# Kernel tuning notes

Hardware: AMD Instinct MI355X
Metric: run time of the kernel (lower is better)

Reference implementation:

```python
import jax, jax.numpy as jnp
import numpy as np

N = 131072      # number of nodes / samples
IN_DIM = 128    # input_dim
H = 128         # hidden_dim
OUT_DIM = 10    # output_dim


def setup_inputs() -> dict:
    key = jax.random.key(0)
    ks = jax.random.split(key, 20)
    s = 0.05
    def rn(k, shape):
        return jax.random.normal(k, shape, jnp.float32) * s
    return {
        "x": jax.random.normal(ks[0], (N, IN_DIM), jnp.float32),
        # GRU layer 1 (seq_len=1, h0=0 => weight_hh contributes nothing; only b_hh matters)
        "w_ih_f1": rn(ks[1], (3 * H, IN_DIM)), "b_ih_f1": rn(ks[2], (3 * H,)), "b_hh_f1": rn(ks[3], (3 * H,)),
        "w_ih_b1": rn(ks[4], (3 * H, IN_DIM)), "b_ih_b1": rn(ks[5], (3 * H,)), "b_hh_b1": rn(ks[6], (3 * H,)),
        # GRU layer 2 (input 2H)
        "w_ih_f2": rn(ks[7], (3 * H, 2 * H)), "b_ih_f2": rn(ks[8], (3 * H,)), "b_hh_f2": rn(ks[9], (3 * H,)),
        "w_ih_b2": rn(ks[10], (3 * H, 2 * H)), "b_ih_b2": rn(ks[11], (3 * H,)), "b_hh_b2": rn(ks[12], (3 * H,)),
        # GCNConv layers
        "w_g1": rn(ks[13], (2 * H, 128)), "b_g1": rn(ks[14], (128,)),
        "w_g2": rn(ks[15], (128, 64)), "b_g2": rn(ks[16], (64,)),
        # final fc
        "w_fc": rn(ks[17], (64, OUT_DIM)), "b_fc": rn(ks[18], (OUT_DIM,)),
    }


def _gru_cell_zero(x, w_ih, b_ih, b_hh):
    # PyTorch GRU cell with h_prev = 0: h' = (1 - z) * n_gate
    gi = x @ w_ih.T + b_ih                    # [n, 3H]
    ir, iz, inn = jnp.split(gi, 3, axis=-1)
    hr, hz, hn = jnp.split(b_hh, 3)
    r = jax.nn.sigmoid(ir + hr)
    z = jax.nn.sigmoid(iz + hz)
    ng = jnp.tanh(inn + r * hn)
    return (1.0 - z) * ng


def _gcn(x, w, b, sources, targets, n):
    # PyG GCNConv: D^{-1/2}(A+I)D^{-1/2} X W + b, self-loops already in edge lists
    xw = x @ w                                 # [n, out]
    deg = jax.ops.segment_sum(jnp.ones(sources.shape[0], x.dtype), targets, num_segments=n)
    dinv = jax.lax.rsqrt(deg)
    norm = dinv[sources] * dinv[targets]       # [E]
    msg = norm[:, None] * xw[sources]          # gather
    return jax.ops.segment_sum(msg, targets, num_segments=n) + b  # scatter-add


def reference(x, w_ih_f1, b_ih_f1, b_hh_f1, w_ih_b1, b_ih_b1, b_hh_b1,
              w_ih_f2, b_ih_f2, b_hh_f2, w_ih_b2, b_ih_b2, b_hh_b2,
              w_g1, b_g1, w_g2, b_g2, w_fc, b_fc):
    n = x.shape[0]
    # seq_len = 1 => bidirectional GRU output is [fwd_cell(x); bwd_cell(x)]
    h1 = jnp.concatenate([_gru_cell_zero(x, w_ih_f1, b_ih_f1, b_hh_f1),
                          _gru_cell_zero(x, w_ih_b1, b_ih_b1, b_hh_b1)], axis=-1)
    h2 = jnp.concatenate([_gru_cell_zero(h1, w_ih_f2, b_ih_f2, b_hh_f2),
                          _gru_cell_zero(h1, w_ih_b2, b_ih_b2, b_hh_b2)], axis=-1)
    # chain graph, both directions, plus self loops (GCNConv adds them)
    src = jnp.arange(n - 1)
    dst = jnp.arange(1, n)
    ar = jnp.arange(n)
    sources = jnp.concatenate([src, dst, ar])
    targets = jnp.concatenate([dst, src, ar])
    g1 = _gcn(h2, w_g1, b_g1, sources, targets, n)   # dropout is identity in eval
    g2 = _gcn(g1, w_g2, b_g2, sources, targets, n)
    return g2 @ w_fc + b_fc
```

## Files before the change

kernel.cpp:

```cpp
#include <hip/hip_runtime.h>
#include <stdint.h>

#define N_NODES 131072
#define HDIM 128

typedef __bf16 bf16x8 __attribute__((ext_vector_type(8)));
typedef float f32x4 __attribute__((ext_vector_type(4)));
typedef unsigned short us8 __attribute__((ext_vector_type(8)));
typedef unsigned short ushort_t;

__device__ __forceinline__ float bf2f(ushort_t u) {
    union { float f; uint32_t i; } v; v.i = ((uint32_t)u) << 16; return v.f;
}
__device__ __forceinline__ ushort_t f2bf(float f) {
    union { float f; uint32_t i; } v; v.f = f;
    uint32_t i = v.i;
    return (ushort_t)((i + 0x7FFFu + ((i >> 16) & 1u)) >> 16);
}

__device__ __forceinline__ void gll16(const ushort_t* g, ushort_t* l) {
    __builtin_amdgcn_global_load_lds(
        (const __attribute__((address_space(1))) uint32_t*)g,
        (__attribute__((address_space(3))) uint32_t*)l, 16, 0, 0);
}

__device__ __forceinline__ bf16x8 ldsw(const ushort_t* base, int R, int g) {
    return *(const bf16x8*)&base[R * 64 + (((g - R) & 7) << 3)];
}

__device__ __forceinline__ float fsig(float x) {
    return __builtin_amdgcn_rcpf(1.0f + __expf(-x));
}
__device__ __forceinline__ float ftanh(float y) {
    float yc = fminf(fmaxf(y, -15.0f), 15.0f);
    float e = __expf(2.0f * yc);
    return (e - 1.0f) * __builtin_amdgcn_rcpf(e + 1.0f);
}

template<int NC>
__device__ __forceinline__ void swz(int b, int& m, int& c) {
    int mhi = b / (8 * NC);
    int rem = b - mhi * (8 * NC);
    c = rem >> 3;
    m = mhi * 8 + (rem & 7);
}

__global__ __launch_bounds__(256) void prep_weights(
    const float* __restrict__ w_f1, const float* __restrict__ w_b1,
    const float* __restrict__ w_f2, const float* __restrict__ w_b2,
    ushort_t* __restrict__ PWF1, ushort_t* __restrict__ PWB1,
    ushort_t* __restrict__ PWF2, ushort_t* __restrict__ PWB2)
{
    int idx = blockIdx.x * 256 + threadIdx.x;
    if (idx < 49152) {
        PWF1[idx] = f2bf(w_f1[idx]);
    } else if (idx < 98304) {
        int j = idx - 49152;  PWB1[j] = f2bf(w_b1[j]);
    } else if (idx < 196608) {
        int j = idx - 98304;  PWF2[j] = f2bf(w_f2[j]);
    } else if (idx < 294912) {
        int j = idx - 196608; PWB2[j] = f2bf(w_b2[j]);
    }
}

__global__ __launch_bounds__(256) void prep_M(
    const float* __restrict__ w_g1, const float* __restrict__ b_g1,
    const float* __restrict__ w_g2, const float* __restrict__ b_g2,
    const float* __restrict__ w_fc, const float* __restrict__ b_fc,
    ushort_t* __restrict__ M16, float* __restrict__ cc)
{
    __shared__ float T1[128][10];
    const int t = threadIdx.x;
    if (t < 128) {
        #pragma unroll
        for (int j = 0; j < 10; ++j) {
            float s = 0.0f;
            for (int k3 = 0; k3 < 64; ++k3) s += w_g2[t * 64 + k3] * w_fc[k3 * 10 + j];
            T1[t][j] = s;
        }
    }
    __syncthreads();
    float m[10];
    #pragma unroll
    for (int j = 0; j < 10; ++j) {
        float s = 0.0f;
        for (int k2 = 0; k2 < 128; ++k2) s += w_g1[t * 128 + k2] * T1[k2][j];
        m[j] = s;
    }
    #pragma unroll
    for (int j = 0; j < 16; ++j)
        M16[j * 256 + t] = (j < 10) ? f2bf(m[j]) : (ushort_t)0;
    if (t < 10) {
        float s1 = 0.0f;
        for (int k2 = 0; k2 < 128; ++k2) s1 += b_g1[k2] * T1[k2][t];
        cc[t] = s1;
        float s2 = 0.0f;
        for (int k3 = 0; k3 < 64; ++k3) s2 += b_g2[k3] * w_fc[k3 * 10 + t];
        cc[16 + t] = s2 + b_fc[t];
    }
}

__global__ __launch_bounds__(256) void xconv(
    const float* __restrict__ x, ushort_t* __restrict__ xb)
{
    int idx = blockIdx.x * 256 + threadIdx.x;
    const float* s = x + (size_t)idx * 8;
    float4 f0 = ((const float4*)s)[0];
    float4 f1 = ((const float4*)s)[1];
    us8 t;
    t[0] = f2bf(f0.x); t[1] = f2bf(f0.y); t[2] = f2bf(f0.z); t[3] = f2bf(f0.w);
    t[4] = f2bf(f1.x); t[5] = f2bf(f1.y); t[6] = f2bf(f1.z); t[7] = f2bf(f1.w);
    *(us8*)&xb[(size_t)idx * 8] = t;
}

template<int K>
__global__ __launch_bounds__(256, 5) void gru_gemm2(
    const ushort_t* __restrict__ A,
    const ushort_t* __restrict__ Wf,
    const ushort_t* __restrict__ Wb,
    const float* __restrict__ bi_f, const float* __restrict__ bh_f,
    const float* __restrict__ bi_b, const float* __restrict__ bh_b,
    ushort_t* __restrict__ Hout)
{
    __shared__ ushort_t As[128 * 64];
    __shared__ ushort_t Bs[96 * 64];
    const int tid = threadIdx.x;
    int mt, comb;
    swz<8>(blockIdx.x, mt, comb);
    const int m0 = mt * 128;
    const int dir = comb >> 2;
    const int j0 = (comb & 3) * 32;
    const ushort_t* W = dir ? Wb : Wf;
    const float* b_ih = dir ? bi_b : bi_f;
    const float* b_hh = dir ? bh_b : bh_f;
    const int coloff = dir << 7;

    const int wv = tid >> 6, lane = tid & 63;
    const int lr = lane & 15, lq = lane >> 4;
    const int tr = tid >> 3, tc = tid & 7;
    const int sc = ((tr + tc) & 7) << 3;

    f32x4 acc[3][2][2];
    #pragma unroll
    for (int g = 0; g < 3; ++g)
        #pragma unroll
        for (int rt = 0; rt < 2; ++rt)
            #pragma unroll
            for (int ct = 0; ct < 2; ++ct)
                #pragma unroll
                for (int e = 0; e < 4; ++e) acc[g][rt][ct][e] = 0.0f;

    for (int t = 0; t < K / 64; ++t) {
        const int k0 = t * 64;
        const ushort_t* ga = A + (size_t)(m0 + tr) * K + k0 + sc;
        #pragma unroll
        for (int i = 0; i < 4; ++i)
            gll16(ga + (size_t)i * 32 * K, &As[(i * 256 + tid) * 8]);
        #pragma unroll
        for (int i = 0; i < 3; ++i) {
            int wr = (i << 7) + j0 + tr;
            gll16(W + (size_t)wr * K + k0 + sc, &Bs[(i * 256 + tid) * 8]);
        }
        __syncthreads();
        #pragma unroll
        for (int kk = 0; kk < 64; kk += 32) {
            const int g8 = (kk >> 3) + lq;
            bf16x8 a0 = ldsw(As, wv * 32 + lr, g8);
            bf16x8 a1 = ldsw(As, wv * 32 + 16 + lr, g8);
            #pragma unroll
            for (int g = 0; g < 3; ++g) {
                #pragma unroll
                for (int ct = 0; ct < 2; ++ct) {
                    bf16x8 b = ldsw(Bs, g * 32 + ct * 16 + lr, g8);
                    acc[g][0][ct] = __builtin_amdgcn_mfma_f32_16x16x32_bf16(a0, b, acc[g][0][ct], 0, 0, 0);
                    acc[g][1][ct] = __builtin_amdgcn_mfma_f32_16x16x32_bf16(a1, b, acc[g][1][ct], 0, 0, 0);
                }
            }
        }
        __syncthreads();
    }

    #pragma unroll
    for (int ct = 0; ct < 2; ++ct) {
        const int j = j0 + ct * 16 + lr;
        const float br  = b_ih[j] + b_hh[j];
        const float bz  = b_ih[HDIM + j] + b_hh[HDIM + j];
        const float bn  = b_ih[2 * HDIM + j];
        const float bhn = b_hh[2 * HDIM + j];
        #pragma unroll
        for (int rt = 0; rt < 2; ++rt) {
            #pragma unroll
            for (int r = 0; r < 4; ++r) {
                const int row = m0 + wv * 32 + rt * 16 + lq * 4 + r;
                float rg = fsig(acc[0][rt][ct][r] + br);
                float zg = fsig(acc[1][rt][ct][r] + bz);
                float ng = ftanh(acc[2][rt][ct][r] + bn + rg * bhn);
                Hout[(size_t)row * 256 + coloff + j] = f2bf((1.0f - zg) * ng);
            }
        }
    }
}

__global__ __launch_bounds__(256, 5) void zgemm(
    const ushort_t* __restrict__ A,
    const ushort_t* __restrict__ M16,
    float* __restrict__ Zc)
{
    __shared__ ushort_t As[128 * 64];
    const int tid = threadIdx.x;
    const int m0 = blockIdx.x * 128;
    const int wv = tid >> 6, lane = tid & 63;
    const int lr = lane & 15, lq = lane >> 4;
    const int tr = tid >> 3, tc = tid & 7;
    const int sc = ((tr + tc) & 7) << 3;

    bf16x8 bfrag[8];
    #pragma unroll
    for (int s = 0; s < 8; ++s)
        bfrag[s] = *(const bf16x8*)&M16[lr * 256 + s * 32 + lq * 8];

    f32x4 acc[2];
    #pragma unroll
    for (int e = 0; e < 4; ++e) { acc[0][e] = 0.0f; acc[1][e] = 0.0f; }

    for (int t = 0; t < 4; ++t) {
        const int k0 = t * 64;
        const ushort_t* ga = A + (size_t)(m0 + tr) * 256 + k0 + sc;
        #pragma unroll
        for (int i = 0; i < 4; ++i)
            gll16(ga + (size_t)i * 32 * 256, &As[(i * 256 + tid) * 8]);
        __syncthreads();
        #pragma unroll
        for (int kk = 0; kk < 64; kk += 32) {
            const int g8 = (kk >> 3) + lq;
            bf16x8 a0 = ldsw(As, wv * 32 + lr, g8);
            bf16x8 a1 = ldsw(As, wv * 32 + 16 + lr, g8);
            bf16x8 b = bfrag[t * 2 + (kk >> 5)];
            acc[0] = __builtin_amdgcn_mfma_f32_16x16x32_bf16(a0, b, acc[0], 0, 0, 0);
            acc[1] = __builtin_amdgcn_mfma_f32_16x16x32_bf16(a1, b, acc[1], 0, 0, 0);
        }
        __syncthreads();
    }

    if (lr < 10) {
        #pragma unroll
        for (int rt = 0; rt < 2; ++rt)
            #pragma unroll
            for (int r = 0; r < 4; ++r) {
                int row = m0 + wv * 32 + rt * 16 + lq * 4 + r;
                Zc[(size_t)row * 10 + lr] = acc[rt][r];
            }
    }
}

__device__ __forceinline__ float dcoef(int i) {
    return (i == 0 || i == N_NODES - 1) ? 0.70710678118654752f : 0.57735026918962576f;
}
template<int FIN>
__global__ __launch_bounds__(256) void stencil10(
    const float* __restrict__ in, float* __restrict__ out,
    const float* __restrict__ cc)
{
    int idx = blockIdx.x * 256 + threadIdx.x;
    int i = idx >> 4, c = idx & 15;
    if (c >= 10) return;
    float di = dcoef(i);
    float s = di * in[(size_t)i * 10 + c];
    float dsum = di;
    if (i > 0)           { float dm = dcoef(i - 1); s += dm * in[(size_t)(i - 1) * 10 + c]; dsum += dm; }
    if (i < N_NODES - 1) { float dp = dcoef(i + 1); s += dp * in[(size_t)(i + 1) * 10 + c]; dsum += dp; }
    float r = di * s;
    if (FIN) r += di * dsum * cc[c] + cc[16 + c];
    out[(size_t)i * 10 + c] = r;
}

extern "C" void kernel_launch(void* const* d_in, const int* in_sizes, int n_in,
                              void* d_out, int out_size, void* d_ws, size_t ws_size,
                              hipStream_t stream) {
    const float* x     = (const float*)d_in[0];
    const float* w_f1  = (const float*)d_in[1];
    const float* bi_f1 = (const float*)d_in[2];
    const float* bh_f1 = (const float*)d_in[3];
    const float* w_b1  = (const float*)d_in[4];
    const float* bi_b1 = (const float*)d_in[5];
    const float* bh_b1 = (const float*)d_in[6];
    const float* w_f2  = (const float*)d_in[7];
    const float* bi_f2 = (const float*)d_in[8];
    const float* bh_f2 = (const float*)d_in[9];
    const float* w_b2  = (const float*)d_in[10];
    const float* bi_b2 = (const float*)d_in[11];
    const float* bh_b2 = (const float*)d_in[12];
    const float* w_g1  = (const float*)d_in[13];
    const float* b_g1  = (const float*)d_in[14];
    const float* w_g2  = (const float*)d_in[15];
    const float* b_g2  = (const float*)d_in[16];
    const float* w_fc  = (const float*)d_in[17];
    const float* b_fc  = (const float*)d_in[18];

    char* ws = (char*)d_ws;
    ushort_t* h1   = (ushort_t*)(ws);
    ushort_t* xb   = (ushort_t*)(ws + 67108864);
    ushort_t* h2   = (ushort_t*)(ws + 67108864);
    float*    Zc   = (float*)(ws);
    float*    u    = (float*)(ws + 8388608);
    ushort_t* PWF1 = (ushort_t*)(ws + 134217728);
    ushort_t* PWB1 = PWF1 + 49152;
    ushort_t* PWF2 = PWB1 + 49152;
    ushort_t* PWB2 = PWF2 + 98304;
    ushort_t* M16  = PWB2 + 98304;
    float*    cc   = (float*)(M16 + 4096);

    prep_weights<<<1152, 256, 0, stream>>>(w_f1, w_b1, w_f2, w_b2,
                                           PWF1, PWB1, PWF2, PWB2);
    prep_M<<<1, 256, 0, stream>>>(w_g1, b_g1, w_g2, b_g2, w_fc, b_fc, M16, cc);
    xconv<<<N_NODES * 16 / 256, 256, 0, stream>>>(x, xb);

    gru_gemm2<128><<<N_NODES / 128 * 8, 256, 0, stream>>>(
        xb, PWF1, PWB1, bi_f1, bh_f1, bi_b1, bh_b1, h1);
    gru_gemm2<256><<<N_NODES / 128 * 8, 256, 0, stream>>>(
        h1, PWF2, PWB2, bi_f2, bh_f2, bi_b2, bh_b2, h2);

    zgemm<<<N_NODES / 128, 256, 0, stream>>>(h2, M16, Zc);
    stencil10<0><<<N_NODES * 16 / 256, 256, 0, stream>>>(Zc, u, cc);
    stencil10<1><<<N_NODES * 16 / 256, 256, 0, stream>>>(u, (float*)d_out, cc);
}
```

Measured before the change: 336.1 us.

## Drop LDS staging in GEMMs, fuse two stencils, vectorize prep_M

The GRU and z GEMMs stop staging tiles in shared memory through global_load_lds plus barriers. Each lane now loads its MFMA fragments straight from global memory and relies on L1/L2 for reuse. The two stencil passes are merged into one 5-point kernel, which removes the intermediate buffer and a launch. prep_M caches w_fc in LDS and uses float4 row loads. Direct global fragment loads can cost more memory traffic and latency because tiles are no longer shared across waves.

```diff
diff --git a/kernel.cpp b/kernel.cpp
--- a/kernel.cpp
+++ b/kernel.cpp
@@ -16,16 +16,6 @@
     union { float f; uint32_t i; } v; v.f = f;
     uint32_t i = v.i;
     return (ushort_t)((i + 0x7FFFu + ((i >> 16) & 1u)) >> 16);
-}
-
-__device__ __forceinline__ void gll16(const ushort_t* g, ushort_t* l) {
-    __builtin_amdgcn_global_load_lds(
-        (const __attribute__((address_space(1))) uint32_t*)g,
-        (__attribute__((address_space(3))) uint32_t*)l, 16, 0, 0);
-}
-
-__device__ __forceinline__ bf16x8 ldsw(const ushort_t* base, int R, int g) {
-    return *(const bf16x8*)&base[R * 64 + (((g - R) & 7) << 3)];
 }
 
 __device__ __forceinline__ float fsig(float x) {
@@ -69,23 +59,39 @@
     const float* __restrict__ w_fc, const float* __restrict__ b_fc,
     ushort_t* __restrict__ M16, float* __restrict__ cc)
 {
+    __shared__ float wfc_s[640];
     __shared__ float T1[128][10];
     const int t = threadIdx.x;
+    for (int i = t; i < 640; i += 256) wfc_s[i] = w_fc[i];
+    __syncthreads();
     if (t < 128) {
-        #pragma unroll
-        for (int j = 0; j < 10; ++j) {
-            float s = 0.0f;
-            for (int k3 = 0; k3 < 64; ++k3) s += w_g2[t * 64 + k3] * w_fc[k3 * 10 + j];
-            T1[t][j] = s;
+        float s[10];
+        #pragma unroll
+        for (int j = 0; j < 10; ++j) s[j] = 0.0f;
+        const float4* row = (const float4*)(w_g2 + t * 64);
+        #pragma unroll
+        for (int k4 = 0; k4 < 16; ++k4) {
+            float4 v = row[k4];
+            #pragma unroll
+            for (int j = 0; j < 10; ++j)
+                s[j] += v.x * wfc_s[(k4 * 4 + 0) * 10 + j] + v.y * wfc_s[(k4 * 4 + 1) * 10 + j]
+                      + v.z * wfc_s[(k4 * 4 + 2) * 10 + j] + v.w * wfc_s[(k4 * 4 + 3) * 10 + j];
         }
+        #pragma unroll
+        for (int j = 0; j < 10; ++j) T1[t][j] = s[j];
     }
     __syncthreads();
     float m[10];
     #pragma unroll
-    for (int j = 0; j < 10; ++j) {
-        float s = 0.0f;
-        for (int k2 = 0; k2 < 128; ++k2) s += w_g1[t * 128 + k2] * T1[k2][j];
-        m[j] = s;
+    for (int j = 0; j < 10; ++j) m[j] = 0.0f;
+    const float4* row1 = (const float4*)(w_g1 + t * 128);
+    #pragma unroll 4
+    for (int k4 = 0; k4 < 32; ++k4) {
+        float4 v = row1[k4];
+        #pragma unroll
+        for (int j = 0; j < 10; ++j)
+            m[j] += v.x * T1[k4 * 4 + 0][j] + v.y * T1[k4 * 4 + 1][j]
+                  + v.z * T1[k4 * 4 + 2][j] + v.w * T1[k4 * 4 + 3][j];
     }
     #pragma unroll
     for (int j = 0; j < 16; ++j)
@@ -95,7 +101,7 @@
         for (int k2 = 0; k2 < 128; ++k2) s1 += b_g1[k2] * T1[k2][t];
         cc[t] = s1;
         float s2 = 0.0f;
-        for (int k3 = 0; k3 < 64; ++k3) s2 += b_g2[k3] * w_fc[k3 * 10 + t];
+        for (int k3 = 0; k3 < 64; ++k3) s2 += b_g2[k3] * wfc_s[k3 * 10 + t];
         cc[16 + t] = s2 + b_fc[t];
     }
 }
@@ -114,7 +120,7 @@
 }
 
 template<int K>
-__global__ __launch_bounds__(256, 5) void gru_gemm2(
+__global__ __launch_bounds__(256) void gru_gemm3(
     const ushort_t* __restrict__ A,
     const ushort_t* __restrict__ Wf,
     const ushort_t* __restrict__ Wb,
@@ -122,8 +128,6 @@
     const float* __restrict__ bi_b, const float* __restrict__ bh_b,
     ushort_t* __restrict__ Hout)
 {
-    __shared__ ushort_t As[128 * 64];
-    __shared__ ushort_t Bs[96 * 64];
     const int tid = threadIdx.x;
     int mt, comb;
     swz<8>(blockIdx.x, mt, comb);
@@ -137,8 +141,10 @@
 
     const int wv = tid >> 6, lane = tid & 63;
     const int lr = lane & 15, lq = lane >> 4;
-    const int tr = tid >> 3, tc = tid & 7;
-    const int sc = ((tr + tc) & 7) << 3;
+
+    const ushort_t* a0p = A + (size_t)(m0 + wv * 32 + lr) * K + lq * 8;
+    const ushort_t* a1p = a0p + (size_t)16 * K;
+    const ushort_t* b00 = W + (size_t)(j0 + lr) * K + lq * 8;
 
     f32x4 acc[3][2][2];
     #pragma unroll
@@ -150,34 +156,19 @@
                 #pragma unroll
                 for (int e = 0; e < 4; ++e) acc[g][rt][ct][e] = 0.0f;
 
-    for (int t = 0; t < K / 64; ++t) {
-        const int k0 = t * 64;
-        const ushort_t* ga = A + (size_t)(m0 + tr) * K + k0 + sc;
-        #pragma unroll
-        for (int i = 0; i < 4; ++i)
-            gll16(ga + (size_t)i * 32 * K, &As[(i * 256 + tid) * 8]);
-        #pragma unroll
-        for (int i = 0; i < 3; ++i) {
-            int wr = (i << 7) + j0 + tr;
-            gll16(W + (size_t)wr * K + k0 + sc, &Bs[(i * 256 + tid) * 8]);
-        }
-        __syncthreads();
-        #pragma unroll
-        for (int kk = 0; kk < 64; kk += 32) {
-            const int g8 = (kk >> 3) + lq;
-            bf16x8 a0 = ldsw(As, wv * 32 + lr, g8);
-            bf16x8 a1 = ldsw(As, wv * 32 + 16 + lr, g8);
-            #pragma unroll
-            for (int g = 0; g < 3; ++g) {
-                #pragma unroll
-                for (int ct = 0; ct < 2; ++ct) {
-                    bf16x8 b = ldsw(Bs, g * 32 + ct * 16 + lr, g8);
-                    acc[g][0][ct] = __builtin_amdgcn_mfma_f32_16x16x32_bf16(a0, b, acc[g][0][ct], 0, 0, 0);
-                    acc[g][1][ct] = __builtin_amdgcn_mfma_f32_16x16x32_bf16(a1, b, acc[g][1][ct], 0, 0, 0);
-                }
+    #pragma unroll 4
+    for (int kk = 0; kk < K; kk += 32) {
+        bf16x8 a0 = *(const bf16x8*)(a0p + kk);
+        bf16x8 a1 = *(const bf16x8*)(a1p + kk);
+        #pragma unroll
+        for (int g = 0; g < 3; ++g) {
+            #pragma unroll
+            for (int ct = 0; ct < 2; ++ct) {
+                bf16x8 b = *(const bf16x8*)(b00 + (size_t)(g * 128 + ct * 16) * K + kk);
+                acc[g][0][ct] = __builtin_amdgcn_mfma_f32_16x16x32_bf16(a0, b, acc[g][0][ct], 0, 0, 0);
+                acc[g][1][ct] = __builtin_amdgcn_mfma_f32_16x16x32_bf16(a1, b, acc[g][1][ct], 0, 0, 0);
             }
         }
-        __syncthreads();
     }
 
     #pragma unroll
@@ -201,45 +192,34 @@
     }
 }
 
-__global__ __launch_bounds__(256, 5) void zgemm(
+__global__ __launch_bounds__(256) void zgemm(
     const ushort_t* __restrict__ A,
     const ushort_t* __restrict__ M16,
     float* __restrict__ Zc)
 {
-    __shared__ ushort_t As[128 * 64];
     const int tid = threadIdx.x;
     const int m0 = blockIdx.x * 128;
     const int wv = tid >> 6, lane = tid & 63;
     const int lr = lane & 15, lq = lane >> 4;
-    const int tr = tid >> 3, tc = tid & 7;
-    const int sc = ((tr + tc) & 7) << 3;
 
     bf16x8 bfrag[8];
     #pragma unroll
     for (int s = 0; s < 8; ++s)
         bfrag[s] = *(const bf16x8*)&M16[lr * 256 + s * 32 + lq * 8];
 
+    const ushort_t* a0p = A + (size_t)(m0 + wv * 32 + lr) * 256 + lq * 8;
+    const ushort_t* a1p = a0p + 16 * 256;
+
     f32x4 acc[2];
     #pragma unroll
     for (int e = 0; e < 4; ++e) { acc[0][e] = 0.0f; acc[1][e] = 0.0f; }
 
-    for (int t = 0; t < 4; ++t) {
-        const int k0 = t * 64;
-        const ushort_t* ga = A + (size_t)(m0 + tr) * 256 + k0 + sc;
-        #pragma unroll
-        for (int i = 0; i < 4; ++i)
-            gll16(ga + (size_t)i * 32 * 256, &As[(i * 256 + tid) * 8]);
-        __syncthreads();
-        #pragma unroll
-        for (int kk = 0; kk < 64; kk += 32) {
-            const int g8 = (kk >> 3) + lq;
-            bf16x8 a0 = ldsw(As, wv * 32 + lr, g8);
-            bf16x8 a1 = ldsw(As, wv * 32 + 16 + lr, g8);
-            bf16x8 b = bfrag[t * 2 + (kk >> 5)];
-            acc[0] = __builtin_amdgcn_mfma_f32_16x16x32_bf16(a0, b, acc[0], 0, 0, 0);
-            acc[1] = __builtin_amdgcn_mfma_f32_16x16x32_bf16(a1, b, acc[1], 0, 0, 0);
-        }
-        __syncthreads();
+    #pragma unroll
+    for (int s = 0; s < 8; ++s) {
+        bf16x8 a0 = *(const bf16x8*)(a0p + s * 32);
+        bf16x8 a1 = *(const bf16x8*)(a1p + s * 32);
+        acc[0] = __builtin_amdgcn_mfma_f32_16x16x32_bf16(a0, bfrag[s], acc[0], 0, 0, 0);
+        acc[1] = __builtin_amdgcn_mfma_f32_16x16x32_bf16(a1, bfrag[s], acc[1], 0, 0, 0);
     }
 
     if (lr < 10) {
@@ -256,22 +236,31 @@
 __device__ __forceinline__ float dcoef(int i) {
     return (i == 0 || i == N_NODES - 1) ? 0.70710678118654752f : 0.57735026918962576f;
 }
-template<int FIN>
-__global__ __launch_bounds__(256) void stencil10(
-    const float* __restrict__ in, float* __restrict__ out,
+__global__ __launch_bounds__(256) void st5(
+    const float* __restrict__ z, float* __restrict__ out,
     const float* __restrict__ cc)
 {
     int idx = blockIdx.x * 256 + threadIdx.x;
     int i = idx >> 4, c = idx & 15;
     if (c >= 10) return;
-    float di = dcoef(i);
-    float s = di * in[(size_t)i * 10 + c];
-    float dsum = di;
-    if (i > 0)           { float dm = dcoef(i - 1); s += dm * in[(size_t)(i - 1) * 10 + c]; dsum += dm; }
-    if (i < N_NODES - 1) { float dp = dcoef(i + 1); s += dp * in[(size_t)(i + 1) * 10 + c]; dsum += dp; }
-    float r = di * s;
-    if (FIN) r += di * dsum * cc[c] + cc[16 + c];
-    out[(size_t)i * 10 + c] = r;
+    float d_i = dcoef(i);
+    float accv = 0.0f, dsum = d_i;
+    #pragma unroll
+    for (int oj = -1; oj <= 1; ++oj) {
+        int j = i + oj;
+        if (j < 0 || j >= N_NODES) continue;
+        float dj = dcoef(j);
+        if (oj != 0) dsum += dj;
+        float wj = 0.0f;
+        #pragma unroll
+        for (int ok = -1; ok <= 1; ++ok) {
+            int k = j + ok;
+            if (k < 0 || k >= N_NODES) continue;
+            wj += dcoef(k) * z[(size_t)k * 10 + c];
+        }
+        accv += dj * dj * wj;
+    }
+    out[(size_t)i * 10 + c] = d_i * accv + d_i * dsum * cc[c] + cc[16 + c];
 }
 
 extern "C" void kernel_launch(void* const* d_in, const int* in_sizes, int n_in,
@@ -302,7 +291,6 @@
     ushort_t* xb   = (ushort_t*)(ws + 67108864);
     ushort_t* h2   = (ushort_t*)(ws + 67108864);
     float*    Zc   = (float*)(ws);
-    float*    u    = (float*)(ws + 8388608);
     ushort_t* PWF1 = (ushort_t*)(ws + 134217728);
     ushort_t* PWB1 = PWF1 + 49152;
     ushort_t* PWF2 = PWB1 + 49152;
@@ -315,12 +303,11 @@
     prep_M<<<1, 256, 0, stream>>>(w_g1, b_g1, w_g2, b_g2, w_fc, b_fc, M16, cc);
     xconv<<<N_NODES * 16 / 256, 256, 0, stream>>>(x, xb);
 
-    gru_gemm2<128><<<N_NODES / 128 * 8, 256, 0, stream>>>(
+    gru_gemm3<128><<<N_NODES / 128 * 8, 256, 0, stream>>>(
         xb, PWF1, PWB1, bi_f1, bh_f1, bi_b1, bh_b1, h1);
-    gru_gemm2<256><<<N_NODES / 128 * 8, 256, 0, stream>>>(
+    gru_gemm3<256><<<N_NODES / 128 * 8, 256, 0, stream>>>(
         h1, PWF2, PWB2, bi_f2, bh_f2, bi_b2, bh_b2, h2);
 
     zgemm<<<N_NODES / 128, 256, 0, stream>>>(h2, M16, Zc);
-    stencil10<0><<<N_NODES * 16 / 256, 256, 0, stream>>>(Zc, u, cc);
-    stencil10<1><<<N_NODES * 16 / 256, 256, 0, stream>>>(u, (float*)d_out, cc);
-}
+    st5<<<N_NODES * 16 / 256, 256, 0, stream>>>(Zc, (float*)d_out, cc);
+}
```

After: 540.8 us. +60.9%, slower.
